# Kernel optimization log

Hardware: AMD Instinct MI355X
Metric: run time of the kernel (lower is better)

Reference implementation:

```python
import math
import jax, jax.numpy as jnp
import numpy as np

NUM_HEADS = 12
DIM = 1536
HEAD_DIM = DIM // NUM_HEADS  # 128
MAX_ATTN = 5632              # max_attention_size for window_size=(-1,-1)
EPS = 1e-6


def rmsnorm(x, g, eps=EPS):
    v = jnp.mean(jnp.square(x.astype(jnp.float32)), axis=-1, keepdims=True)
    return (x.astype(jnp.float32) * jax.lax.rsqrt(v + eps)).astype(x.dtype) * g


def causal_rope_apply(x, theta, start_frame, f, h, w):
    # x: [B, S, N, D] with S = f*h*w; theta: [1024, D//2] angles.
    b, s, n, d = x.shape
    c = d // 2
    ct = c - 2 * (c // 3)  # temporal rotary dims (22)
    ch = c // 3            # spatial rotary dims (21)
    ang = jnp.concatenate([
        jnp.broadcast_to(theta[start_frame:start_frame + f, :ct][:, None, None, :], (f, h, w, ct)),
        jnp.broadcast_to(theta[:h, ct:ct + ch][None, :, None, :], (f, h, w, ch)),
        jnp.broadcast_to(theta[:w, ct + ch:ct + 2 * ch][None, None, :, :], (f, h, w, ch)),
    ], axis=-1).reshape(s, c)
    cos = jnp.cos(ang)[None, :, None, :]  # [1, S, 1, c]
    sin = jnp.sin(ang)[None, :, None, :]
    xp = x.reshape(b, s, n, c, 2)
    xr, xi = xp[..., 0], xp[..., 1]
    out_r = xr * cos - xi * sin
    out_i = xr * sin + xi * cos
    return jnp.stack([out_r, out_i], axis=-1).reshape(b, s, n, d)


def setup_inputs() -> dict:
    key = jax.random.key(0)
    ks = jax.random.split(key, 12)
    B, F, H, W = 1, 2, 30, 52
    S = F * H * W  # 3120
    CACHE_LEN = 15600
    wscale = 0.02
    inp = {
        "x": jax.random.normal(ks[0], (B, S, DIM), jnp.float32),
        "freqs_theta": jax.random.uniform(ks[1], (1024, HEAD_DIM // 2), jnp.float32, 0.0, 2.0 * np.pi),
        "cache_k": jax.random.normal(ks[2], (B, CACHE_LEN, NUM_HEADS, HEAD_DIM), jnp.float32),
        "cache_v": jax.random.normal(ks[3], (B, CACHE_LEN, NUM_HEADS, HEAD_DIM), jnp.float32),
        "wq": jax.random.normal(ks[4], (DIM, DIM), jnp.float32) * wscale,
        "bq": jnp.zeros((DIM,), jnp.float32),
        "wk": jax.random.normal(ks[5], (DIM, DIM), jnp.float32) * wscale,
        "bk": jnp.zeros((DIM,), jnp.float32),
        "wv": jax.random.normal(ks[6], (DIM, DIM), jnp.float32) * wscale,
        "bv": jnp.zeros((DIM,), jnp.float32),
        "wo": jax.random.normal(ks[7], (DIM, DIM), jnp.float32) * wscale,
        "bo": jnp.zeros((DIM,), jnp.float32),
        "gq": jnp.ones((DIM,), jnp.float32),
        "gk": jnp.ones((DIM,), jnp.float32),
        "grid_f": F, "grid_h": H, "grid_w": W,
        "current_start": 7800,       # 5 frames already generated
        "global_end_index": 7800,
        "local_end_index": 7800,
    }
    return inp


def reference(x, freqs_theta, cache_k, cache_v, wq, bq, wk, bk, wv, bv, wo, bo,
              gq, gk, grid_f, grid_h, grid_w, current_start, global_end_index,
              local_end_index):
    B, S, D = x.shape
    N, Hd = NUM_HEADS, HEAD_DIM
    # qkv projections with RMS q/k norm (applied on full dim before head split)
    q = rmsnorm(x @ wq.T + bq, gq).reshape(B, S, N, Hd)
    k = rmsnorm(x @ wk.T + bk, gk).reshape(B, S, N, Hd)
    v = (x @ wv.T + bv).reshape(B, S, N, Hd)

    frame_seqlen = grid_h * grid_w
    start_frame = current_start // frame_seqlen
    rq = causal_rope_apply(q, freqs_theta, start_frame, grid_f, grid_h, grid_w)
    rk = causal_rope_apply(k, freqs_theta, start_frame, grid_f, grid_h, grid_w)

    # KV-cache scatter (static indices)
    current_end = current_start + S
    local_end = local_end_index + current_end - global_end_index
    local_start = local_end - S
    cache_k = cache_k.at[:, local_start:local_end].set(rk)
    cache_v = cache_v.at[:, local_start:local_end].set(v)

    # windowed attention over last MAX_ATTN cached tokens
    win_start = max(0, local_end - MAX_ATTN)
    kwin = cache_k[:, win_start:local_end]
    vwin = cache_v[:, win_start:local_end]
    scale = 1.0 / math.sqrt(Hd)
    scores = jnp.einsum('bqnd,bknd->bnqk', rq, kwin) * scale
    p = jax.nn.softmax(scores, axis=-1)
    o = jnp.einsum('bnqk,bknd->bqnd', p, vwin).reshape(B, S, D)
    return o @ wo.T + bo
```

## Files before the change

### kernel.cpp

```cpp
#include <hip/hip_runtime.h>

#define DIM 1536
#define NHEADS 12
#define HD 128
#define MAX_ATTN_WIN 5632
#define RMS_EPS 1e-6f
#define KWROWS 5632
#define NT_MAX 88
#define TILE_ELEMS 8192
#define KSTEPS 48
#define AREG 4096
#define BREG 8192

typedef unsigned short ushortT;
typedef __bf16 bf16x8 __attribute__((ext_vector_type(8)));
typedef float f32x4 __attribute__((ext_vector_type(4)));
typedef ushortT ushx8 __attribute__((ext_vector_type(8)));

__device__ __forceinline__ ushortT bf16r(float x) {
    union { float f; unsigned u; } v; v.f = x;
    unsigned r = v.u + 0x7FFFu + ((v.u >> 16) & 1u);
    return (ushortT)(r >> 16);
}
__device__ __forceinline__ ushx8 pack8(float4 a, float4 b) {
    ushx8 u;
    u[0] = bf16r(a.x); u[1] = bf16r(a.y); u[2] = bf16r(a.z); u[3] = bf16r(a.w);
    u[4] = bf16r(b.x); u[5] = bf16r(b.y); u[6] = bf16r(b.z); u[7] = bf16r(b.w);
    return u;
}

__device__ __forceinline__ void gload_lds16(const void* g, void* l) {
    typedef const __attribute__((address_space(1))) unsigned int GU;
    typedef __attribute__((address_space(3))) unsigned int LU;
    __builtin_amdgcn_global_load_lds((GU*)(unsigned long long)g,
                                     (LU*)(unsigned long long)l, 16, 0, 0);
}

__global__ __launch_bounds__(256)
void pack_a_kernel(const float* __restrict__ X, ushortT* __restrict__ Ap,
                   int M, int Mpad)
{
    int idx = blockIdx.x * 256 + threadIdx.x;
    if (idx >= Mpad * 192) return;
    int row = idx / 192, ch = idx - row * 192;
    int ks = ch >> 2, c = ch & 3;
    int mb = row >> 6, r = row & 63;
    ushx8 uh, ul;
    if (row < M) {
        const float* p = X + (size_t)row * DIM + (ch << 3);
        float4 a = *(const float4*)p;
        float4 b2 = *(const float4*)(p + 4);
        float xs[8] = {a.x, a.y, a.z, a.w, b2.x, b2.y, b2.z, b2.w};
        #pragma unroll
        for (int j = 0; j < 8; ++j) {
            ushortT hh = bf16r(xs[j]);
            union { unsigned u; float f; } w; w.u = ((unsigned)hh) << 16;
            uh[j] = hh; ul[j] = bf16r(xs[j] - w.f);
        }
    } else {
        #pragma unroll
        for (int j = 0; j < 8; ++j) { uh[j] = 0; ul[j] = 0; }
    }
    size_t base = (size_t)(mb * KSTEPS + ks) * AREG
                + r * 32 + ((c ^ ((r >> 1) & 3)) << 3);
    *(ushx8*)&Ap[base] = uh;
    *(ushx8*)&Ap[base + 2048] = ul;
}

__global__ __launch_bounds__(256)
void pack_b_kernel(const float* __restrict__ W, ushortT* __restrict__ Bp)
{
    int idx = blockIdx.x * 256 + threadIdx.x;
    if (idx >= DIM * 192) return;
    int row = idx / 192, ch = idx - row * 192;
    int ks = ch >> 2, c = ch & 3;
    int nb = row >> 7, rn = row & 127;
    const float* p = W + (size_t)row * DIM + (ch << 3);
    float4 a = *(const float4*)p;
    float4 b2 = *(const float4*)(p + 4);
    float xs[8] = {a.x, a.y, a.z, a.w, b2.x, b2.y, b2.z, b2.w};
    ushx8 uh, ul;
    #pragma unroll
    for (int j = 0; j < 8; ++j) {
        ushortT hh = bf16r(xs[j]);
        union { unsigned u; float f; } w; w.u = ((unsigned)hh) << 16;
        uh[j] = hh; ul[j] = bf16r(xs[j] - w.f);
    }
    size_t base = (size_t)(nb * KSTEPS + ks) * BREG
                + rn * 32 + ((c ^ ((rn >> 1) & 3)) << 3);
    *(ushx8*)&Bp[base] = uh;
    *(ushx8*)&Bp[base + 4096] = ul;
}

template<int MODE>
__global__ __launch_bounds__(256, 3)
void gemm_fast_kernel(const ushortT* __restrict__ Ap, const ushortT* __restrict__ Bp,
                      const float* __restrict__ bias, float* __restrict__ C,
                      ushortT* __restrict__ vwout, int M, int nmb,
                      const int* __restrict__ p_cs, const int* __restrict__ p_ge,
                      const int* __restrict__ p_le)
{
    __shared__ __align__(16) ushortT As[2][AREG];
    __shared__ __align__(16) ushortT Bs[2][BREG];

    const int tid = threadIdx.x;
    const int wid = tid >> 6, lane = tid & 63;
    const int lo = lane & 15, hi = lane >> 4;
    const int wm = wid >> 1, wn = wid & 1;

    const int nwg = nmb * (DIM / 128);
    const int orig = (int)blockIdx.x;
    const int xcd = orig & 7, linb = orig >> 3;
    const int qd = nwg >> 3, rr2 = nwg & 7;
    const int wg = (xcd < rr2 ? xcd * (qd + 1) : rr2 * (qd + 1) + (xcd - rr2) * qd) + linb;
    const int nb = wg / nmb, mb = wg - nb * nmb;
    const int m0 = mb << 6, n0 = nb << 7;

    f32x4 acc[2][4];
    #pragma unroll
    for (int i = 0; i < 2; ++i)
        #pragma unroll
        for (int j = 0; j < 4; ++j) acc[i][j] = (f32x4)(0.f);

    const ushortT* Asrc = Ap + (size_t)mb * (KSTEPS * AREG);
    const ushortT* Bsrc = Bp + (size_t)nb * (KSTEPS * BREG);
    const int lofs = lane << 3;
    const int aBase0 = (wid << 10) + lofs;
    const int aBase1 = aBase0 + 512;
    const int bBase  = (wid << 11) + lofs;

    gload_lds16(Asrc + aBase0, &As[0][aBase0]);
    gload_lds16(Asrc + aBase1, &As[0][aBase1]);
    #pragma unroll
    for (int i = 0; i < 4; ++i)
        gload_lds16(Bsrc + bBase + (i << 9), &Bs[0][bBase + (i << 9)]);

    const int cOff = ((hi ^ ((lo >> 1) & 3)) << 3);

    for (int ks = 0; ks < KSTEPS; ++ks) {
        const int b = ks & 1;
        __syncthreads();
        if (ks + 1 < KSTEPS) {
            const ushortT* as1 = Asrc + ((size_t)(ks + 1) << 12);
            const ushortT* bs1 = Bsrc + ((size_t)(ks + 1) << 13);
            gload_lds16(as1 + aBase0, &As[b ^ 1][aBase0]);
            gload_lds16(as1 + aBase1, &As[b ^ 1][aBase1]);
            #pragma unroll
            for (int i = 0; i < 4; ++i)
                gload_lds16(bs1 + bBase + (i << 9), &Bs[b ^ 1][bBase + (i << 9)]);
        }

        bf16x8 aH[2], aL[2];
        #pragma unroll
        for (int mf = 0; mf < 2; ++mf) {
            int r = (wm << 5) + (mf << 4) + lo;
            aH[mf] = *(const bf16x8*)&As[b][r * 32 + cOff];
            aL[mf] = *(const bf16x8*)&As[b][r * 32 + cOff + 2048];
        }
        #pragma unroll
        for (int nf = 0; nf < 4; ++nf) {
            int rn = (wn << 6) + (nf << 4) + lo;
            bf16x8 bH = *(const bf16x8*)&Bs[b][rn * 32 + cOff];
            bf16x8 bL = *(const bf16x8*)&Bs[b][rn * 32 + cOff + 4096];
            #pragma unroll
            for (int mf = 0; mf < 2; ++mf) {
                acc[mf][nf] = __builtin_amdgcn_mfma_f32_16x16x32_bf16(aH[mf], bH, acc[mf][nf], 0, 0, 0);
                acc[mf][nf] = __builtin_amdgcn_mfma_f32_16x16x32_bf16(aL[mf], bH, acc[mf][nf], 0, 0, 0);
                acc[mf][nf] = __builtin_amdgcn_mfma_f32_16x16x32_bf16(aH[mf], bL, acc[mf][nf], 0, 0, 0);
            }
        }
    }

    if (MODE == 0) {
        #pragma unroll
        for (int mf = 0; mf < 2; ++mf) {
            #pragma unroll
            for (int reg = 0; reg < 4; ++reg) {
                int gm = m0 + (wm << 5) + (mf << 4) + (hi << 2) + reg;
                if (gm < M) {
                    #pragma unroll
                    for (int nf = 0; nf < 4; ++nf) {
                        int gn = n0 + (wn << 6) + (nf << 4) + lo;
                        C[(size_t)gm * DIM + gn] = acc[mf][nf][reg] + bias[gn];
                    }
                }
            }
        }
    } else {
        const int S = M;
        const int local_end = p_le[0] + (p_cs[0] + S) - p_ge[0];
        int win_start = local_end - MAX_ATTN_WIN; if (win_start < 0) win_start = 0;
        const int vbase = (local_end - S) - win_start;
        #pragma unroll
        for (int mf = 0; mf < 2; ++mf) {
            #pragma unroll
            for (int reg = 0; reg < 4; ++reg) {
                int gm = m0 + (wm << 5) + (mf << 4) + (hi << 2) + reg;
                if (gm < M) {
                    #pragma unroll
                    for (int nf = 0; nf < 4; ++nf) {
                        int gn = n0 + (wn << 6) + (nf << 4) + lo;
                        int h2 = gn >> 7, d = gn & 127;
                        int pos = vbase + gm;
                        int tt = pos >> 6, w = pos & 63;
                        int swz = (((w >> 3) ^ (d & 7)) << 3) | (w & 7);
                        vwout[((size_t)h2 * NT_MAX + tt) * TILE_ELEMS + ((size_t)d << 6) + swz] =
                            bf16r(acc[mf][nf][reg] + bias[gn]);
                    }
                }
            }
        }
    }
}

__global__ __launch_bounds__(256)
void rmsnorm_rope_kernel(float* __restrict__ qbuf, float* __restrict__ kbuf,
                         const float* __restrict__ gq, const float* __restrict__ gk,
                         const float* __restrict__ theta,
                         const int* __restrict__ p_gh, const int* __restrict__ p_gw,
                         const int* __restrict__ p_cs, int S)
{
    const int s = blockIdx.x;
    float* row = ((blockIdx.y == 0) ? qbuf : kbuf) + (size_t)s * DIM;
    const float* g = (blockIdx.y == 0) ? gq : gk;
    const int tid = threadIdx.x;

    float v[6];
    #pragma unroll
    for (int i = 0; i < 6; ++i) v[i] = row[tid * 6 + i];
    float ss = 0.f;
    #pragma unroll
    for (int i = 0; i < 6; ++i) ss += v[i] * v[i];
    #pragma unroll
    for (int off = 32; off > 0; off >>= 1) ss += __shfl_xor(ss, off, 64);

    __shared__ float red[4];
    if ((tid & 63) == 0) red[tid >> 6] = ss;
    __syncthreads();
    float tot = red[0] + red[1] + red[2] + red[3];
    float rs = rsqrtf(tot * (1.0f / DIM) + RMS_EPS);

    const int H = p_gh[0], W = p_gw[0];
    const int fs = p_cs[0] / (H * W);
    const int fr = s / (H * W);
    const int rem = s - fr * (H * W);
    const int hh = rem / W;
    const int ww = rem - hh * W;

    #pragma unroll
    for (int pi = 0; pi < 3; ++pi) {
        int p = tid * 3 + pi;
        int j = p & 63;
        float xr = v[pi * 2]     * rs * g[tid * 6 + pi * 2];
        float xi = v[pi * 2 + 1] * rs * g[tid * 6 + pi * 2 + 1];
        int rowi = (j < 22) ? (fs + fr) : ((j < 43) ? hh : ww);
        float ang = theta[rowi * 64 + j];
        float sn, cs;
        sincosf(ang, &sn, &cs);
        row[tid * 6 + pi * 2]     = xr * cs - xi * sn;
        row[tid * 6 + pi * 2 + 1] = xr * sn + xi * cs;
    }
}

__global__ __launch_bounds__(256)
void pack_k_kernel(const float* __restrict__ cache_k, const float* __restrict__ k_lin,
                   ushortT* __restrict__ kw,
                   const int* __restrict__ p_cs, const int* __restrict__ p_ge,
                   const int* __restrict__ p_le, int S)
{
    const int kt = blockIdx.x, h = blockIdx.y;
    const int local_end = p_le[0] + (p_cs[0] + S) - p_ge[0];
    int win_start = local_end - MAX_ATTN_WIN; if (win_start < 0) win_start = 0;
    const int L = local_end - win_start;
    const int cpart = (local_end - S) - win_start;

    #pragma unroll
    for (int i = 0; i < 4; ++i) {
        int cid = (i << 8) + threadIdx.x;
        int r = cid >> 4, c = cid & 15;
        int pos = (kt << 6) + r;
        ushx8 u;
        if (pos < L) {
            const float* src = (pos < cpart)
                ? &cache_k[(size_t)(win_start + pos) * DIM + h * HD + (c << 3)]
                : &k_lin[(size_t)(pos - cpart) * DIM + h * HD + (c << 3)];
            float4 a = *(const float4*)src;
            float4 b = *(const float4*)(src + 4);
            u = pack8(a, b);
        } else {
            #pragma unroll
            for (int j = 0; j < 8; ++j) u[j] = 0;
        }
        *(ushx8*)&kw[(size_t)h * (KWROWS * HD) + (size_t)pos * HD + ((c ^ (r & 15)) << 3)] = u;
    }
}

__global__ __launch_bounds__(256)
void pack_v_cache_kernel(const float* __restrict__ cache_v, ushortT* __restrict__ vw,
                         const int* __restrict__ p_cs, const int* __restrict__ p_ge,
                         const int* __restrict__ p_le, int S)
{
    const int kt = blockIdx.x, h = blockIdx.y;
    const int local_end = p_le[0] + (p_cs[0] + S) - p_ge[0];
    int win_start = local_end - MAX_ATTN_WIN; if (win_start < 0) win_start = 0;
    const int L = local_end - win_start;
    const int cpart = (local_end - S) - win_start;
    const int tbase = kt << 6;
    if (tbase >= cpart && tbase + 64 <= L) return;

    __shared__ float tile[64 * 132];
    #pragma unroll
    for (int i = 0; i < 8; ++i) {
        int cid = (i << 8) + threadIdx.x;
        int r = cid >> 5, fc = cid & 31;
        int pos = tbase + r;
        float4 vv = (pos < cpart)
            ? *(const float4*)&cache_v[(size_t)(win_start + pos) * DIM + h * HD + (fc << 2)]
            : make_float4(0.f, 0.f, 0.f, 0.f);
        *(float4*)&tile[r * 132 + (fc << 2)] = vv;
    }
    __syncthreads();
    #pragma unroll
    for (int i = 0; i < 4; ++i) {
        int cid = (i << 8) + threadIdx.x;
        int d = cid >> 3, kc = cid & 7;
        int kglob = tbase + (kc << 3);
        ushx8 u;
        #pragma unroll
        for (int j = 0; j < 8; ++j)
            u[j] = bf16r(tile[((kc << 3) + j) * 132 + d]);
        size_t base = ((size_t)h * NT_MAX + kt) * TILE_ELEMS + ((size_t)d << 6)
                    + ((size_t)((kc ^ (d & 7)) << 3));
        if (kglob + 8 <= cpart) {
            *(ushx8*)&vw[base] = u;
        } else {
            #pragma unroll
            for (int j = 0; j < 8; ++j) {
                int pos = kglob + j;
                if (pos < cpart)      vw[base + j] = u[j];
                else if (pos >= L)    vw[base + j] = 0;
            }
        }
    }
}

__global__ __launch_bounds__(256, 2)
void attn_mfma4_kernel(const float* __restrict__ q_lin,
                       const ushortT* __restrict__ kw, const ushortT* __restrict__ vw,
                       float* __restrict__ obuf,
                       const int* __restrict__ p_cs, const int* __restrict__ p_ge,
                       const int* __restrict__ p_le, int S, int nqb)
{
    __shared__ __align__(16) ushortT Ks[2][TILE_ELEMS];
    __shared__ __align__(16) ushortT Vs[2][TILE_ELEMS];
    __shared__ __align__(16) ushortT Ps[4096];

    const int tid = threadIdx.x;
    const int wid = tid >> 6, lane = tid & 63;
    const int lo = lane & 15, hi = lane >> 4;

    const int nwg = nqb * NHEADS;
    const int orig = (int)blockIdx.x;
    const int xcd = orig & 7, linb = orig >> 3;
    const int qd = nwg >> 3, rr = nwg & 7;
    const int wg = (xcd < rr ? xcd * (qd + 1) : rr * (qd + 1) + (xcd - rr) * qd) + linb;
    const int h = wg / nqb;
    const int q0 = (wg - h * nqb) << 6;

    const int local_end = p_le[0] + (p_cs[0] + S) - p_ge[0];
    int win_start = local_end - MAX_ATTN_WIN; if (win_start < 0) win_start = 0;
    const int L = local_end - win_start;
    const int ntiles = (L + 63) >> 6;

    bf16x8 aQ[4];
    {
        int q = q0 + (wid << 4) + lo;
        if (q < S) {
            const float* qp = q_lin + (size_t)q * DIM + h * HD + (hi << 3);
            #pragma unroll
            for (int ks = 0; ks < 4; ++ks) {
                float4 a = *(const float4*)&qp[ks * 32];
                float4 b = *(const float4*)&qp[ks * 32 + 4];
                ushx8 u = pack8(a, b);
                aQ[ks] = *(bf16x8*)&u;
            }
        } else {
            ushx8 z;
            #pragma unroll
            for (int j = 0; j < 8; ++j) z[j] = 0;
            #pragma unroll
            for (int ks = 0; ks < 4; ++ks) aQ[ks] = *(bf16x8*)&z;
        }
    }

    f32x4 Oa[8];
    float lsum[4];
    #pragma unroll
    for (int i = 0; i < 8; ++i) Oa[i] = (f32x4)(0.f);
    #pragma unroll
    for (int i = 0; i < 4; ++i) lsum[i] = 0.f;

    const ushortT* kwp = kw + (size_t)h * (NT_MAX * TILE_ELEMS);
    const ushortT* vwp = vw + (size_t)h * (NT_MAX * TILE_ELEMS);
    const float scale = 0.08838834764831845f;
    const int pbase = wid << 10;
    const int sbase = (wid << 11) + (lane << 3);

    #pragma unroll
    for (int i = 0; i < 4; ++i) {
        gload_lds16(kwp + sbase + (i << 9), &Ks[0][sbase + (i << 9)]);
        gload_lds16(vwp + sbase + (i << 9), &Vs[0][sbase + (i << 9)]);
    }

    for (int t = 0; t < ntiles; ++t) {
        const int b = t & 1;
        __syncthreads();

        if (t + 1 < ntiles) {
            const ushortT* ksrc = kwp + ((size_t)(t + 1) << 13);
            const ushortT* vsrc = vwp + ((size_t)(t + 1) << 13);
            ushortT* kdst = &Ks[b ^ 1][0];
            ushortT* vdst = &Vs[b ^ 1][0];
            #pragma unroll
            for (int i = 0; i < 4; ++i) {
                gload_lds16(ksrc + sbase + (i << 9), kdst + sbase + (i << 9));
                gload_lds16(vsrc + sbase + (i << 9), vdst + sbase + (i << 9));
            }
        }

        f32x4 Sa[4];
        #pragma unroll
        for (int nt = 0; nt < 4; ++nt) Sa[nt] = (f32x4)(0.f);
        #pragma unroll
        for (int nt = 0; nt < 4; ++nt) {
            const int kr = (nt << 4) + lo;
            #pragma unroll
            for (int ks = 0; ks < 4; ++ks) {
                bf16x8 bF = *(const bf16x8*)&Ks[b][kr * 128 + ((((ks << 2) + hi) ^ (kr & 15)) << 3)];
                Sa[nt] = __builtin_amdgcn_mfma_f32_16x16x32_bf16(aQ[ks], bF, Sa[nt], 0, 0, 0);
            }
        }

        const bool tail = (((t + 1) << 6) > L);
        #pragma unroll
        for (int nt = 0; nt < 4; ++nt) {
            #pragma unroll
            for (int reg = 0; reg < 4; ++reg) {
                float sv = Sa[nt][reg] * scale - 20.f;
                if (tail) {
                    int kg = (t << 6) + (nt << 4) + lo;
                    if (kg >= L) sv = -1e30f;
                }
                float p = __expf(sv);
                lsum[reg] += p;
                Sa[nt][reg] = p;
            }
        }

        #pragma unroll
        for (int nt = 0; nt < 4; ++nt) {
            #pragma unroll
            for (int reg = 0; reg < 4; ++reg) {
                int r = (hi << 2) + reg;
                int cc = (nt << 1) + (lo >> 3);
                Ps[pbase + (r << 6) + ((cc ^ (r & 7)) << 3) + (lo & 7)] = bf16r(Sa[nt][reg]);
            }
        }
        bf16x8 pF[2];
        #pragma unroll
        for (int ks = 0; ks < 2; ++ks)
            pF[ks] = *(const bf16x8*)&Ps[pbase + (lo << 6) + ((((ks << 2) + hi) ^ (lo & 7)) << 3)];

        #pragma unroll
        for (int nto = 0; nto < 8; ++nto) {
            const int d = (nto << 4) + lo;
            #pragma unroll
            for (int ks = 0; ks < 2; ++ks) {
                bf16x8 vF = *(const bf16x8*)&Vs[b][(d << 6) + ((((ks << 2) + hi) ^ (d & 7)) << 3)];
                Oa[nto] = __builtin_amdgcn_mfma_f32_16x16x32_bf16(pF[ks], vF, Oa[nto], 0, 0, 0);
            }
        }
    }

    #pragma unroll
    for (int reg = 0; reg < 4; ++reg) {
        #pragma unroll
        for (int off = 1; off < 16; off <<= 1)
            lsum[reg] += __shfl_xor(lsum[reg], off, 64);
    }
    #pragma unroll
    for (int reg = 0; reg < 4; ++reg) {
        int q = q0 + (wid << 4) + (hi << 2) + reg;
        if (q < S) {
            float inv = 1.f / lsum[reg];
            #pragma unroll
            for (int nto = 0; nto < 8; ++nto)
                obuf[(size_t)q * DIM + h * HD + (nto << 4) + lo] = Oa[nto][reg] * inv;
        }
    }
}

extern "C" void kernel_launch(void* const* d_in, const int* in_sizes, int n_in,
                              void* d_out, int out_size, void* d_ws, size_t ws_size,
                              hipStream_t stream)
{
    const float* x       = (const float*)d_in[0];
    const float* theta   = (const float*)d_in[1];
    const float* cache_k = (const float*)d_in[2];
    const float* cache_v = (const float*)d_in[3];
    const float* wq = (const float*)d_in[4];
    const float* bq = (const float*)d_in[5];
    const float* wk = (const float*)d_in[6];
    const float* bk = (const float*)d_in[7];
    const float* wv = (const float*)d_in[8];
    const float* bv = (const float*)d_in[9];
    const float* wo = (const float*)d_in[10];
    const float* bo = (const float*)d_in[11];
    const float* gq = (const float*)d_in[12];
    const float* gk = (const float*)d_in[13];
    const int* p_gh = (const int*)d_in[15];
    const int* p_gw = (const int*)d_in[16];
    const int* p_cs = (const int*)d_in[17];
    const int* p_ge = (const int*)d_in[18];
    const int* p_le = (const int*)d_in[19];

    const int S = in_sizes[0] / DIM;
    const int nmb = (S + 63) / 64;
    const int Mpad = nmb * 64;

    float* q_lin = (float*)d_ws;
    float* k_lin = q_lin + (size_t)S * DIM;
    float* o_buf = k_lin;
    ushortT* Ap  = (ushortT*)(k_lin + (size_t)S * DIM);
    ushortT* kw  = Ap;
    ushortT* vw  = Ap + (size_t)nmb * KSTEPS * AREG;
    ushortT* Bp0 = vw + (size_t)NHEADS * NT_MAX * TILE_ELEMS;
    ushortT* Bp1 = Bp0 + (size_t)NHEADS * KSTEPS * BREG;

    dim3 blk(256);
    const int nwgG = nmb * (DIM / 128);
    const int packA_grid = (Mpad * 192 + 255) / 256;
    const int packB_grid = (DIM * 192 + 255) / 256;

    pack_a_kernel<<<packA_grid, blk, 0, stream>>>(x, Ap, S, Mpad);
    pack_b_kernel<<<packB_grid, blk, 0, stream>>>(wq, Bp0);
    gemm_fast_kernel<0><<<nwgG, blk, 0, stream>>>(Ap, Bp0, bq, q_lin, nullptr,
                                                  S, nmb, p_cs, p_ge, p_le);
    pack_b_kernel<<<packB_grid, blk, 0, stream>>>(wk, Bp1);
    gemm_fast_kernel<0><<<nwgG, blk, 0, stream>>>(Ap, Bp1, bk, k_lin, nullptr,
                                                  S, nmb, p_cs, p_ge, p_le);
    pack_b_kernel<<<packB_grid, blk, 0, stream>>>(wv, Bp0);
    gemm_fast_kernel<1><<<nwgG, blk, 0, stream>>>(Ap, Bp0, bv, nullptr, vw,
                                                  S, nmb, p_cs, p_ge, p_le);

    rmsnorm_rope_kernel<<<dim3(S, 2), blk, 0, stream>>>(q_lin, k_lin, gq, gk, theta,
                                                        p_gh, p_gw, p_cs, S);

    pack_k_kernel<<<dim3(NT_MAX, NHEADS), blk, 0, stream>>>(cache_k, k_lin, kw,
                                                            p_cs, p_ge, p_le, S);
    pack_v_cache_kernel<<<dim3(NT_MAX, NHEADS), blk, 0, stream>>>(cache_v, vw,
                                                                  p_cs, p_ge, p_le, S);

    const int nqb = (S + 63) / 64;
    attn_mfma4_kernel<<<dim3(nqb * NHEADS), blk, 0, stream>>>(
        q_lin, kw, vw, o_buf, p_cs, p_ge, p_le, S, nqb);

    pack_b_kernel<<<packB_grid, blk, 0, stream>>>(wo, Bp1);
    pack_a_kernel<<<packA_grid, blk, 0, stream>>>(o_buf, Ap, S, Mpad);
    gemm_fast_kernel<0><<<nwgG, blk, 0, stream>>>(Ap, Bp1, bo, (float*)d_out, nullptr,
                                                  S, nmb, p_cs, p_ge, p_le);
}
```

Baseline: 720.9 us.

## Merge pack/GEMM launches and shrink attention LDS for higher occupancy

Pack kernels for x, wq and wk are merged into one launch, and wv and wo into another. The Q and K projection GEMMs run as one launch with twice the grid, and the K and V cache packers become a single kernel. The attention kernel now single-buffers K, reuses the K buffer for P staging and drops the separate P array, which cuts LDS enough to raise launch bounds from 2 to 3 blocks per CU. K prefetch moves to after the P reads, with extra barriers and an explicit waitcnt. The aim is fewer launch gaps and better occupancy, at the cost of less overlap on K loads and an added sync per tile.

```diff
diff --git a/kernel.cpp b/kernel.cpp
--- a/kernel.cpp
+++ b/kernel.cpp
@@ -36,12 +36,10 @@
                                      (LU*)(unsigned long long)l, 16, 0, 0);
 }
 
-__global__ __launch_bounds__(256)
-void pack_a_kernel(const float* __restrict__ X, ushortT* __restrict__ Ap,
-                   int M, int Mpad)
-{
-    int idx = blockIdx.x * 256 + threadIdx.x;
-    if (idx >= Mpad * 192) return;
+__device__ __forceinline__ void pack_a_body(const float* __restrict__ X,
+                                            ushortT* __restrict__ Ap,
+                                            int M, int idx)
+{
     int row = idx / 192, ch = idx - row * 192;
     int ks = ch >> 2, c = ch & 3;
     int mb = row >> 6, r = row & 63;
@@ -67,11 +65,9 @@
     *(ushx8*)&Ap[base + 2048] = ul;
 }
 
-__global__ __launch_bounds__(256)
-void pack_b_kernel(const float* __restrict__ W, ushortT* __restrict__ Bp)
-{
-    int idx = blockIdx.x * 256 + threadIdx.x;
-    if (idx >= DIM * 192) return;
+__device__ __forceinline__ void pack_b_body(const float* __restrict__ W,
+                                            ushortT* __restrict__ Bp, int idx)
+{
     int row = idx / 192, ch = idx - row * 192;
     int ks = ch >> 2, c = ch & 3;
     int nb = row >> 7, rn = row & 127;
@@ -92,24 +88,55 @@
     *(ushx8*)&Bp[base + 4096] = ul;
 }
 
+__global__ __launch_bounds__(256)
+void pack1_kernel(const float* __restrict__ x, const float* __restrict__ wq,
+                  const float* __restrict__ wk,
+                  ushortT* __restrict__ Ap, ushortT* __restrict__ Bp0,
+                  ushortT* __restrict__ Bp1, int M, int gA, int gB)
+{
+    int b = blockIdx.x;
+    if (b < gA) {
+        pack_a_body(x, Ap, M, b * 256 + threadIdx.x);
+    } else if (b < gA + gB) {
+        pack_b_body(wq, Bp0, (b - gA) * 256 + threadIdx.x);
+    } else {
+        pack_b_body(wk, Bp1, (b - gA - gB) * 256 + threadIdx.x);
+    }
+}
+
+__global__ __launch_bounds__(256)
+void pack2_kernel(const float* __restrict__ wv, const float* __restrict__ wo,
+                  ushortT* __restrict__ Bp0, ushortT* __restrict__ Bp1, int gB)
+{
+    int b = blockIdx.x;
+    if (b < gB) pack_b_body(wv, Bp0, b * 256 + threadIdx.x);
+    else        pack_b_body(wo, Bp1, (b - gB) * 256 + threadIdx.x);
+}
+
+__global__ __launch_bounds__(256)
+void pack_a_kernel(const float* __restrict__ X, ushortT* __restrict__ Ap,
+                   int M, int Mpad)
+{
+    int idx = blockIdx.x * 256 + threadIdx.x;
+    if (idx >= Mpad * 192) return;
+    pack_a_body(X, Ap, M, idx);
+}
+
 template<int MODE>
-__global__ __launch_bounds__(256, 3)
-void gemm_fast_kernel(const ushortT* __restrict__ Ap, const ushortT* __restrict__ Bp,
-                      const float* __restrict__ bias, float* __restrict__ C,
-                      ushortT* __restrict__ vwout, int M, int nmb,
-                      const int* __restrict__ p_cs, const int* __restrict__ p_ge,
-                      const int* __restrict__ p_le)
-{
-    __shared__ __align__(16) ushortT As[2][AREG];
-    __shared__ __align__(16) ushortT Bs[2][BREG];
-
+__device__ __forceinline__
+void gemm_body(const ushortT* __restrict__ Ap, const ushortT* __restrict__ Bp,
+               const float* __restrict__ bias, float* __restrict__ C,
+               ushortT* __restrict__ vwout, int M, int nmb, int orig,
+               const int* __restrict__ p_cs, const int* __restrict__ p_ge,
+               const int* __restrict__ p_le,
+               ushortT (*As)[AREG], ushortT (*Bs)[BREG])
+{
     const int tid = threadIdx.x;
     const int wid = tid >> 6, lane = tid & 63;
     const int lo = lane & 15, hi = lane >> 4;
     const int wm = wid >> 1, wn = wid & 1;
 
     const int nwg = nmb * (DIM / 128);
-    const int orig = (int)blockIdx.x;
     const int xcd = orig & 7, linb = orig >> 3;
     const int qd = nwg >> 3, rr2 = nwg & 7;
     const int wg = (xcd < rr2 ? xcd * (qd + 1) : rr2 * (qd + 1) + (xcd - rr2) * qd) + linb;
@@ -213,6 +240,36 @@
     }
 }
 
+__global__ __launch_bounds__(256, 3)
+void gemm_qk_kernel(const ushortT* __restrict__ Ap,
+                    const ushortT* __restrict__ BpQ, const ushortT* __restrict__ BpK,
+                    const float* __restrict__ bq, const float* __restrict__ bk,
+                    float* __restrict__ Cq, float* __restrict__ Ck,
+                    int M, int nmb, int nwg)
+{
+    __shared__ __align__(16) ushortT As[2][AREG];
+    __shared__ __align__(16) ushortT Bs[2][BREG];
+    int gid = (int)blockIdx.x;
+    if (gid < nwg)
+        gemm_body<0>(Ap, BpQ, bq, Cq, nullptr, M, nmb, gid, nullptr, nullptr, nullptr, As, Bs);
+    else
+        gemm_body<0>(Ap, BpK, bk, Ck, nullptr, M, nmb, gid - nwg, nullptr, nullptr, nullptr, As, Bs);
+}
+
+template<int MODE>
+__global__ __launch_bounds__(256, 3)
+void gemm_single_kernel(const ushortT* __restrict__ Ap, const ushortT* __restrict__ Bp,
+                        const float* __restrict__ bias, float* __restrict__ C,
+                        ushortT* __restrict__ vwout, int M, int nmb,
+                        const int* __restrict__ p_cs, const int* __restrict__ p_ge,
+                        const int* __restrict__ p_le)
+{
+    __shared__ __align__(16) ushortT As[2][AREG];
+    __shared__ __align__(16) ushortT Bs[2][BREG];
+    gemm_body<MODE>(Ap, Bp, bias, C, vwout, M, nmb, (int)blockIdx.x,
+                    p_cs, p_ge, p_le, As, Bs);
+}
+
 __global__ __launch_bounds__(256)
 void rmsnorm_rope_kernel(float* __restrict__ qbuf, float* __restrict__ kbuf,
                          const float* __restrict__ gq, const float* __restrict__ gk,
@@ -263,97 +320,90 @@
 }
 
 __global__ __launch_bounds__(256)
-void pack_k_kernel(const float* __restrict__ cache_k, const float* __restrict__ k_lin,
-                   ushortT* __restrict__ kw,
-                   const int* __restrict__ p_cs, const int* __restrict__ p_ge,
-                   const int* __restrict__ p_le, int S)
-{
-    const int kt = blockIdx.x, h = blockIdx.y;
+void pack_kv_kernel(const float* __restrict__ cache_k, const float* __restrict__ k_lin,
+                    const float* __restrict__ cache_v,
+                    ushortT* __restrict__ kw, ushortT* __restrict__ vw,
+                    const int* __restrict__ p_cs, const int* __restrict__ p_ge,
+                    const int* __restrict__ p_le, int S)
+{
+    const int kt = blockIdx.x;
     const int local_end = p_le[0] + (p_cs[0] + S) - p_ge[0];
     int win_start = local_end - MAX_ATTN_WIN; if (win_start < 0) win_start = 0;
     const int L = local_end - win_start;
     const int cpart = (local_end - S) - win_start;
 
-    #pragma unroll
-    for (int i = 0; i < 4; ++i) {
-        int cid = (i << 8) + threadIdx.x;
-        int r = cid >> 4, c = cid & 15;
-        int pos = (kt << 6) + r;
-        ushx8 u;
-        if (pos < L) {
-            const float* src = (pos < cpart)
-                ? &cache_k[(size_t)(win_start + pos) * DIM + h * HD + (c << 3)]
-                : &k_lin[(size_t)(pos - cpart) * DIM + h * HD + (c << 3)];
-            float4 a = *(const float4*)src;
-            float4 b = *(const float4*)(src + 4);
-            u = pack8(a, b);
-        } else {
-            #pragma unroll
-            for (int j = 0; j < 8; ++j) u[j] = 0;
-        }
-        *(ushx8*)&kw[(size_t)h * (KWROWS * HD) + (size_t)pos * HD + ((c ^ (r & 15)) << 3)] = u;
-    }
-}
-
-__global__ __launch_bounds__(256)
-void pack_v_cache_kernel(const float* __restrict__ cache_v, ushortT* __restrict__ vw,
-                         const int* __restrict__ p_cs, const int* __restrict__ p_ge,
-                         const int* __restrict__ p_le, int S)
-{
-    const int kt = blockIdx.x, h = blockIdx.y;
-    const int local_end = p_le[0] + (p_cs[0] + S) - p_ge[0];
-    int win_start = local_end - MAX_ATTN_WIN; if (win_start < 0) win_start = 0;
-    const int L = local_end - win_start;
-    const int cpart = (local_end - S) - win_start;
-    const int tbase = kt << 6;
-    if (tbase >= cpart && tbase + 64 <= L) return;
-
-    __shared__ float tile[64 * 132];
-    #pragma unroll
-    for (int i = 0; i < 8; ++i) {
-        int cid = (i << 8) + threadIdx.x;
-        int r = cid >> 5, fc = cid & 31;
-        int pos = tbase + r;
-        float4 vv = (pos < cpart)
-            ? *(const float4*)&cache_v[(size_t)(win_start + pos) * DIM + h * HD + (fc << 2)]
-            : make_float4(0.f, 0.f, 0.f, 0.f);
-        *(float4*)&tile[r * 132 + (fc << 2)] = vv;
-    }
-    __syncthreads();
-    #pragma unroll
-    for (int i = 0; i < 4; ++i) {
-        int cid = (i << 8) + threadIdx.x;
-        int d = cid >> 3, kc = cid & 7;
-        int kglob = tbase + (kc << 3);
-        ushx8 u;
-        #pragma unroll
-        for (int j = 0; j < 8; ++j)
-            u[j] = bf16r(tile[((kc << 3) + j) * 132 + d]);
-        size_t base = ((size_t)h * NT_MAX + kt) * TILE_ELEMS + ((size_t)d << 6)
-                    + ((size_t)((kc ^ (d & 7)) << 3));
-        if (kglob + 8 <= cpart) {
-            *(ushx8*)&vw[base] = u;
-        } else {
-            #pragma unroll
-            for (int j = 0; j < 8; ++j) {
-                int pos = kglob + j;
-                if (pos < cpart)      vw[base + j] = u[j];
-                else if (pos >= L)    vw[base + j] = 0;
-            }
-        }
-    }
-}
-
-__global__ __launch_bounds__(256, 2)
-void attn_mfma4_kernel(const float* __restrict__ q_lin,
+    if (blockIdx.y < NHEADS) {
+        const int h = blockIdx.y;
+        #pragma unroll
+        for (int i = 0; i < 4; ++i) {
+            int cid = (i << 8) + threadIdx.x;
+            int r = cid >> 4, c = cid & 15;
+            int pos = (kt << 6) + r;
+            ushx8 u;
+            if (pos < L) {
+                const float* src = (pos < cpart)
+                    ? &cache_k[(size_t)(win_start + pos) * DIM + h * HD + (c << 3)]
+                    : &k_lin[(size_t)(pos - cpart) * DIM + h * HD + (c << 3)];
+                float4 a = *(const float4*)src;
+                float4 b = *(const float4*)(src + 4);
+                u = pack8(a, b);
+            } else {
+                #pragma unroll
+                for (int j = 0; j < 8; ++j) u[j] = 0;
+            }
+            *(ushx8*)&kw[(size_t)h * (KWROWS * HD) + (size_t)pos * HD + ((c ^ (r & 15)) << 3)] = u;
+        }
+    } else {
+        const int h = blockIdx.y - NHEADS;
+        const int tbase = kt << 6;
+        if (tbase >= cpart && tbase + 64 <= L) return;
+
+        __shared__ float tile[64 * 132];
+        #pragma unroll
+        for (int i = 0; i < 8; ++i) {
+            int cid = (i << 8) + threadIdx.x;
+            int r = cid >> 5, fc = cid & 31;
+            int pos = tbase + r;
+            float4 vv = (pos < cpart)
+                ? *(const float4*)&cache_v[(size_t)(win_start + pos) * DIM + h * HD + (fc << 2)]
+                : make_float4(0.f, 0.f, 0.f, 0.f);
+            *(float4*)&tile[r * 132 + (fc << 2)] = vv;
+        }
+        __syncthreads();
+        #pragma unroll
+        for (int i = 0; i < 4; ++i) {
+            int cid = (i << 8) + threadIdx.x;
+            int d = cid >> 3, kc = cid & 7;
+            int kglob = tbase + (kc << 3);
+            ushx8 u;
+            #pragma unroll
+            for (int j = 0; j < 8; ++j)
+                u[j] = bf16r(tile[((kc << 3) + j) * 132 + d]);
+            size_t base = ((size_t)h * NT_MAX + kt) * TILE_ELEMS + ((size_t)d << 6)
+                        + ((size_t)((kc ^ (d & 7)) << 3));
+            if (kglob + 8 <= cpart) {
+                *(ushx8*)&vw[base] = u;
+            } else {
+                #pragma unroll
+                for (int j = 0; j < 8; ++j) {
+                    int pos = kglob + j;
+                    if (pos < cpart)      vw[base + j] = u[j];
+                    else if (pos >= L)    vw[base + j] = 0;
+                }
+            }
+        }
+    }
+}
+
+__global__ __launch_bounds__(256, 3)
+void attn_mfma5_kernel(const float* __restrict__ q_lin,
                        const ushortT* __restrict__ kw, const ushortT* __restrict__ vw,
                        float* __restrict__ obuf,
                        const int* __restrict__ p_cs, const int* __restrict__ p_ge,
                        const int* __restrict__ p_le, int S, int nqb)
 {
-    __shared__ __align__(16) ushortT Ks[2][TILE_ELEMS];
+    __shared__ __align__(16) ushortT Ks[TILE_ELEMS];
     __shared__ __align__(16) ushortT Vs[2][TILE_ELEMS];
-    __shared__ __align__(16) ushortT Ps[4096];
 
     const int tid = threadIdx.x;
     const int wid = tid >> 6, lane = tid & 63;
@@ -403,12 +453,12 @@
     const ushortT* kwp = kw + (size_t)h * (NT_MAX * TILE_ELEMS);
     const ushortT* vwp = vw + (size_t)h * (NT_MAX * TILE_ELEMS);
     const float scale = 0.08838834764831845f;
-    const int pbase = wid << 10;
+    const int pbase = wid << 11;
     const int sbase = (wid << 11) + (lane << 3);
 
     #pragma unroll
     for (int i = 0; i < 4; ++i) {
-        gload_lds16(kwp + sbase + (i << 9), &Ks[0][sbase + (i << 9)]);
+        gload_lds16(kwp + sbase + (i << 9), &Ks[sbase + (i << 9)]);
         gload_lds16(vwp + sbase + (i << 9), &Vs[0][sbase + (i << 9)]);
     }
 
@@ -416,18 +466,6 @@
         const int b = t & 1;
         __syncthreads();
 
-        if (t + 1 < ntiles) {
-            const ushortT* ksrc = kwp + ((size_t)(t + 1) << 13);
-            const ushortT* vsrc = vwp + ((size_t)(t + 1) << 13);
-            ushortT* kdst = &Ks[b ^ 1][0];
-            ushortT* vdst = &Vs[b ^ 1][0];
-            #pragma unroll
-            for (int i = 0; i < 4; ++i) {
-                gload_lds16(ksrc + sbase + (i << 9), kdst + sbase + (i << 9));
-                gload_lds16(vsrc + sbase + (i << 9), vdst + sbase + (i << 9));
-            }
-        }
-
         f32x4 Sa[4];
         #pragma unroll
         for (int nt = 0; nt < 4; ++nt) Sa[nt] = (f32x4)(0.f);
@@ -436,9 +474,19 @@
             const int kr = (nt << 4) + lo;
             #pragma unroll
             for (int ks = 0; ks < 4; ++ks) {
-                bf16x8 bF = *(const bf16x8*)&Ks[b][kr * 128 + ((((ks << 2) + hi) ^ (kr & 15)) << 3)];
+                bf16x8 bF = *(const bf16x8*)&Ks[kr * 128 + ((((ks << 2) + hi) ^ (kr & 15)) << 3)];
                 Sa[nt] = __builtin_amdgcn_mfma_f32_16x16x32_bf16(aQ[ks], bF, Sa[nt], 0, 0, 0);
             }
+        }
+
+        __syncthreads();
+
+        if (t + 1 < ntiles) {
+            const ushortT* vsrc = vwp + ((size_t)(t + 1) << 13);
+            ushortT* vdst = &Vs[b ^ 1][0];
+            #pragma unroll
+            for (int i = 0; i < 4; ++i)
+                gload_lds16(vsrc + sbase + (i << 9), vdst + sbase + (i << 9));
         }
 
         const bool tail = (((t + 1) << 6) > L);
@@ -463,13 +511,23 @@
             for (int reg = 0; reg < 4; ++reg) {
                 int r = (hi << 2) + reg;
                 int cc = (nt << 1) + (lo >> 3);
-                Ps[pbase + (r << 6) + ((cc ^ (r & 7)) << 3) + (lo & 7)] = bf16r(Sa[nt][reg]);
+                Ks[pbase + (r << 6) + ((cc ^ (r & 7)) << 3) + (lo & 7)] = bf16r(Sa[nt][reg]);
             }
         }
         bf16x8 pF[2];
         #pragma unroll
         for (int ks = 0; ks < 2; ++ks)
-            pF[ks] = *(const bf16x8*)&Ps[pbase + (lo << 6) + ((((ks << 2) + hi) ^ (lo & 7)) << 3)];
+            pF[ks] = *(const bf16x8*)&Ks[pbase + (lo << 6) + ((((ks << 2) + hi) ^ (lo & 7)) << 3)];
+
+        asm volatile("s_waitcnt lgkmcnt(0)" ::: "memory");
+        __builtin_amdgcn_sched_barrier(0);
+
+        if (t + 1 < ntiles) {
+            const ushortT* ksrc = kwp + ((size_t)(t + 1) << 13);
+            #pragma unroll
+            for (int i = 0; i < 4; ++i)
+                gload_lds16(ksrc + sbase + (i << 9), &Ks[sbase + (i << 9)]);
+        }
 
         #pragma unroll
         for (int nto = 0; nto < 8; ++nto) {
@@ -539,34 +597,27 @@
 
     dim3 blk(256);
     const int nwgG = nmb * (DIM / 128);
-    const int packA_grid = (Mpad * 192 + 255) / 256;
-    const int packB_grid = (DIM * 192 + 255) / 256;
-
-    pack_a_kernel<<<packA_grid, blk, 0, stream>>>(x, Ap, S, Mpad);
-    pack_b_kernel<<<packB_grid, blk, 0, stream>>>(wq, Bp0);
-    gemm_fast_kernel<0><<<nwgG, blk, 0, stream>>>(Ap, Bp0, bq, q_lin, nullptr,
-                                                  S, nmb, p_cs, p_ge, p_le);
-    pack_b_kernel<<<packB_grid, blk, 0, stream>>>(wk, Bp1);
-    gemm_fast_kernel<0><<<nwgG, blk, 0, stream>>>(Ap, Bp1, bk, k_lin, nullptr,
-                                                  S, nmb, p_cs, p_ge, p_le);
-    pack_b_kernel<<<packB_grid, blk, 0, stream>>>(wv, Bp0);
-    gemm_fast_kernel<1><<<nwgG, blk, 0, stream>>>(Ap, Bp0, bv, nullptr, vw,
-                                                  S, nmb, p_cs, p_ge, p_le);
+    const int gA = (Mpad * 192) / 256;
+    const int gB = (DIM * 192) / 256;
+
+    pack1_kernel<<<gA + 2 * gB, blk, 0, stream>>>(x, wq, wk, Ap, Bp0, Bp1, S, gA, gB);
+    gemm_qk_kernel<<<2 * nwgG, blk, 0, stream>>>(Ap, Bp0, Bp1, bq, bk,
+                                                 q_lin, k_lin, S, nmb, nwgG);
+    pack2_kernel<<<2 * gB, blk, 0, stream>>>(wv, wo, Bp0, Bp1, gB);
+    gemm_single_kernel<1><<<nwgG, blk, 0, stream>>>(Ap, Bp0, bv, nullptr, vw,
+                                                    S, nmb, p_cs, p_ge, p_le);
 
     rmsnorm_rope_kernel<<<dim3(S, 2), blk, 0, stream>>>(q_lin, k_lin, gq, gk, theta,
                                                         p_gh, p_gw, p_cs, S);
 
-    pack_k_kernel<<<dim3(NT_MAX, NHEADS), blk, 0, stream>>>(cache_k, k_lin, kw,
-                                                            p_cs, p_ge, p_le, S);
-    pack_v_cache_kernel<<<dim3(NT_MAX, NHEADS), blk, 0, stream>>>(cache_v, vw,
-                                                                  p_cs, p_ge, p_le, S);
+    pack_kv_kernel<<<dim3(NT_MAX, 2 * NHEADS), blk, 0, stream>>>(
+        cache_k, k_lin, cache_v, kw, vw, p_cs, p_ge, p_le, S);
 
     const int nqb = (S + 63) / 64;
-    attn_mfma4_kernel<<<dim3(nqb * NHEADS), blk, 0, stream>>>(
+    attn_mfma5_kernel<<<dim3(nqb * NHEADS), blk, 0, stream>>>(
         q_lin, kw, vw, o_buf, p_cs, p_ge, p_le, S, nqb);
 
-    pack_b_kernel<<<packB_grid, blk, 0, stream>>>(wo, Bp1);
-    pack_a_kernel<<<packA_grid, blk, 0, stream>>>(o_buf, Ap, S, Mpad);
-    gemm_fast_kernel<0><<<nwgG, blk, 0, stream>>>(Ap, Bp1, bo, (float*)d_out, nullptr,
-                                                  S, nmb, p_cs, p_ge, p_le);
-}
+    pack_a_kernel<<<gA, blk, 0, stream>>>(o_buf, Ap, S, Mpad);
+    gemm_single_kernel<0><<<nwgG, blk, 0, stream>>>(Ap, Bp1, bo, (float*)d_out, nullptr,
+                                                    S, nmb, p_cs, p_ge, p_le);
+}
```

New measurement: 681.2 us. -5.5%, faster.
